# Kernel optimization log

Measured on AMD Instinct MI355X. Metric: run time of the kernel, lower is better.

## Reference

```python
import jax, jax.numpy as jnp
import numpy as np


def setup_inputs() -> dict:
    key = jax.random.key(0)
    ks = jax.random.split(key, 10)
    T, B, I, H, Z = 1024, 512, 128, 256, 1
    s = 0.1  # small init scale for stable recurrence
    return {
        "inputs": jax.random.normal(ks[0], (T, B, I), dtype=jnp.float32),
        "h0": jax.random.normal(ks[1], (B, H), dtype=jnp.float32) * s,
        "c0": jax.random.normal(ks[2], (B, H), dtype=jnp.float32) * s,
        "z0": jax.random.normal(ks[3], (B, Z), dtype=jnp.float32) * s,
        "W_ih": jax.random.normal(ks[4], (4 * H, I + Z), dtype=jnp.float32) * s,
        "W_hh": jax.random.normal(ks[5], (4 * H, H), dtype=jnp.float32) * s,
        "b_ih": jax.random.normal(ks[6], (4 * H,), dtype=jnp.float32) * s,
        "b_hh": jax.random.normal(ks[7], (4 * H,), dtype=jnp.float32) * s,
        "W_fc": jax.random.normal(ks[8], (Z, H), dtype=jnp.float32) * s,
        "b_fc": jax.random.normal(ks[9], (Z,), dtype=jnp.float32) * s,
    }


def reference(inputs, h0, c0, z0, W_ih, W_hh, b_ih, b_hh, W_fc, b_fc):
    def step(carry, x_t):
        h, c, z = carry
        xz = jnp.concatenate([x_t, z], axis=1)  # [B, I+Z]
        gates = xz @ W_ih.T + b_ih + h @ W_hh.T + b_hh  # [B, 4H]
        i_g, f_g, g_g, o_g = jnp.split(gates, 4, axis=1)  # torch gate order i,f,g,o
        i_g = jax.nn.sigmoid(i_g)
        f_g = jax.nn.sigmoid(f_g)
        g_g = jnp.tanh(g_g)
        o_g = jax.nn.sigmoid(o_g)
        c = f_g * c + i_g * g_g
        h = o_g * jnp.tanh(c)
        z = jnp.tanh(h @ W_fc.T + b_fc)  # [B, Z]
        return (h, c, z), z

    (h, c, _), outputs = jax.lax.scan(step, (h0, c0, z0), inputs)
    return outputs, h, c  # outputs: [T, B, Z]
```

## Files before the change

### kernel.cpp

```cpp
#include <hip/hip_runtime.h>
#include <hip/hip_bf16.h>
#include <stdint.h>

#define TT 1024
#define BB 512
#define II 128
#define HH 256
#define NKC 12
#define GSTR 132

typedef __attribute__((ext_vector_type(8))) short bf16x8;
typedef __attribute__((ext_vector_type(4))) float f32x4;
typedef __attribute__((ext_vector_type(4))) uint32_t u32x4;
typedef unsigned long long ull;

__device__ __forceinline__ float fsig(float x)  { return 1.0f / (1.0f + __expf(-x)); }
__device__ __forceinline__ float ftanh(float x) { return 1.0f - 2.0f / (__expf(2.0f * x) + 1.0f); }
__device__ __forceinline__ uint16_t f2bf(float f) {
    return __bfloat16_as_ushort(__float2bfloat16(f));
}
__device__ __forceinline__ float bf2lo(uint32_t w) { return __uint_as_float(w << 16); }
__device__ __forceinline__ float bf2hi(uint32_t w) { return __uint_as_float(w & 0xffff0000u); }

__global__ __launch_bounds__(512, 1) void lstm_kernel(
    const float* __restrict__ x,
    const float* __restrict__ h0, const float* __restrict__ c0,
    const float* __restrict__ z0,
    const float* __restrict__ W_ih, const float* __restrict__ W_hh,
    const float* __restrict__ b_ih, const float* __restrict__ b_hh,
    const float* __restrict__ Wfc, const float* __restrict__ bfc,
    uint32_t* __restrict__ hbF, uint32_t* __restrict__ hbS,
    float* __restrict__ out)
{
    __shared__ __align__(16) uint16_t a_sh[NKC * 4 * 16 * 8];
    __shared__ float g_sh[16 * GSTR];
    __shared__ float zp_sh[8 * 16];

    const int tid  = threadIdx.x;
    const int lane = tid & 63, wv = tid >> 6;
    const int bid  = blockIdx.x;
    const int mm   = bid >> 3;
    const int role = mm & 7, grp = (bid & 7) * 4 + (mm >> 3);
    const int b0   = grp * 16;
    const int arow = tid >> 5, auu = tid & 31;
    const int u_g  = role * 32 + auu;
    const int xc   = (tid & 31) * 4;
    const int grole = wv, grow = lane & 15, gwq = lane >> 4;

    bf16x8 wreg[NKC];
    {
        int lc = wv * 16 + (lane & 15);
        int col = (lc >> 5) * 256 + role * 32 + (lc & 31);
        #pragma unroll
        for (int kc = 0; kc < NKC; ++kc) {
            int k0 = kc * 32 + (lane >> 4) * 8;
            const float* src = (k0 < II) ? &W_ih[(size_t)col * (II + 1) + k0]
                                         : &W_hh[(size_t)col * HH + (k0 - II)];
            bf16x8 wv8;
            #pragma unroll
            for (int j = 0; j < 8; ++j) wv8[j] = (short)f2bf(src[j]);
            wreg[kc] = wv8;
        }
    }

    float bia[4], wzv[4];
    #pragma unroll
    for (int g = 0; g < 4; ++g) {
        int c = g * 256 + u_g;
        bia[g] = b_ih[c] + b_hh[c];
        wzv[g] = W_ih[(size_t)c * (II + 1) + II];
    }
    float wfc8[8];
    #pragma unroll
    for (int j = 0; j < 8; ++j) wfc8[j] = Wfc[grole * 32 + gwq * 8 + j];
    const float wfc  = Wfc[u_g];
    const float bfcs = bfc[0];
    const float z0r  = z0[b0 + arow];
    float c_r = c0[(size_t)(b0 + arow) * HH + u_g];

    {
        const float* hp = h0 + (size_t)(b0 + grow) * HH + grole * 32 + gwq * 8;
        uint4 pw;
        pw.x = (uint32_t)f2bf(hp[0]) | ((uint32_t)f2bf(hp[1]) << 16);
        pw.y = (uint32_t)f2bf(hp[2]) | ((uint32_t)f2bf(hp[3]) << 16);
        pw.z = (uint32_t)f2bf(hp[4]) | ((uint32_t)f2bf(hp[5]) << 16);
        pw.w = (uint32_t)f2bf(hp[6]) | ((uint32_t)f2bf(hp[7]) << 16);
        *(uint4*)&a_sh[(((4 + grole) * 4 + gwq) * 16 + grow) * 8] = pw;
    }
    {
        float4 xv = *(const float4*)&x[(size_t)(b0 + arow) * II + xc];
        int kcx = xc >> 5, gx = (xc >> 3) & 3, jx = xc & 7;
        ushort4 p;
        p.x = f2bf(xv.x); p.y = f2bf(xv.y); p.z = f2bf(xv.z); p.w = f2bf(xv.w);
        *(ushort4*)&a_sh[((kcx * 4 + gx) * 16 + arow) * 8 + jx] = p;
    }

    uint32_t strikes = 0;
    for (int t = 0; t <= TT; ++t) {
        float4 xn = make_float4(0.f, 0.f, 0.f, 0.f);
        if (t + 1 < TT)
            xn = *(const float4*)&x[(size_t)(t + 1) * (BB * II) + (size_t)(b0 + arow) * II + xc];

        if (t > 0 && grole != role) {
            const int par = (t - 1) & 1;
            const size_t gidx = ((((size_t)par * 32 + grp) * 8 + grole) * 16 + grow) * 16
                              + gwq * 4;
            const ull* pF = (const ull*)hbF + gidx;
            const ull* pS = (const ull*)hbS + gidx;
            u32x4 a0, a1;
            uint32_t it = 0;
            const uint32_t cap = (strikes >= 4) ? 64u : (1u << 20);
            const uint32_t tt = (uint32_t)t;
            for (;;) {
                u32x4 f0, f1;
                asm volatile(
                    "global_load_dwordx4 %0, %2, off sc0\n\t"
                    "global_load_dwordx4 %1, %2, off offset:16 sc0\n\t"
                    "s_waitcnt vmcnt(0)"
                    : "=&v"(f0), "=&v"(f1) : "v"(pF) : "memory");
                if (min(min(f0.y, f0.w), min(f1.y, f1.w)) >= tt) { a0 = f0; a1 = f1; break; }
                ++it;
                if ((it & 3) != 0) { __builtin_amdgcn_s_sleep(1); continue; }
                u32x4 s0, s1;
                asm volatile(
                    "global_load_dwordx4 %0, %2, off sc0 sc1\n\t"
                    "global_load_dwordx4 %1, %2, off offset:16 sc0 sc1\n\t"
                    "s_waitcnt vmcnt(0)"
                    : "=&v"(s0), "=&v"(s1) : "v"(pS) : "memory");
                if (min(min(s0.y, s0.w), min(s1.y, s1.w)) >= tt) { a0 = s0; a1 = s1; break; }
                __builtin_amdgcn_s_sleep(1);
                if (it > cap) { ++strikes; a0 = s0; a1 = s1; break; }
            }
            uint32_t w0 = a0.x, w1 = a0.z, w2 = a1.x, w3 = a1.z;
            uint4 pw; pw.x = w0; pw.y = w1; pw.z = w2; pw.w = w3;
            *(uint4*)&a_sh[(((4 + grole) * 4 + gwq) * 16 + grow) * 8] = pw;
            float p = bf2lo(w0) * wfc8[0] + bf2hi(w0) * wfc8[1]
                    + bf2lo(w1) * wfc8[2] + bf2hi(w1) * wfc8[3]
                    + bf2lo(w2) * wfc8[4] + bf2hi(w2) * wfc8[5]
                    + bf2lo(w3) * wfc8[6] + bf2hi(w3) * wfc8[7];
            p += __shfl_xor(p, 16, 64);
            p += __shfl_xor(p, 32, 64);
            if (gwq == 0) zp_sh[grole * 16 + grow] = p;
        }
        __syncthreads();

        if (t == TT) {
            if (role == 0 && tid < 16) {
                float s = bfcs;
                #pragma unroll
                for (int r = 0; r < 8; ++r) s += zp_sh[r * 16 + tid];
                out[(size_t)(TT - 1) * BB + b0 + tid] = ftanh(s);
            }
            break;
        }

        f32x4 acc0 = {0.f, 0.f, 0.f, 0.f}, acc1 = {0.f, 0.f, 0.f, 0.f};
        #pragma unroll
        for (int kc = 0; kc < NKC; kc += 2) {
            bf16x8 a0 = *(const bf16x8*)&a_sh[((kc * 4 + (lane >> 4)) * 16 + (lane & 15)) * 8];
            acc0 = __builtin_amdgcn_mfma_f32_16x16x32_bf16(a0, wreg[kc], acc0, 0, 0, 0);
            bf16x8 a1 = *(const bf16x8*)&a_sh[(((kc + 1) * 4 + (lane >> 4)) * 16 + (lane & 15)) * 8];
            acc1 = __builtin_amdgcn_mfma_f32_16x16x32_bf16(a1, wreg[kc + 1], acc1, 0, 0, 0);
        }
        f32x4 acc = acc0 + acc1;
        {
            int r0 = (lane >> 4) * 4, cb = wv * 16 + (lane & 15);
            #pragma unroll
            for (int i = 0; i < 4; ++i) g_sh[(r0 + i) * GSTR + cb] = acc[i];
        }
        __syncthreads();

        {
            int kcx = xc >> 5, gx = (xc >> 3) & 3, jx = xc & 7;
            ushort4 p;
            p.x = f2bf(xn.x); p.y = f2bf(xn.y); p.z = f2bf(xn.z); p.w = f2bf(xn.w);
            *(ushort4*)&a_sh[((kcx * 4 + gx) * 16 + arow) * 8 + jx] = p;
        }

        float zp_;
        if (t == 0) {
            zp_ = z0r;
        } else {
            float s = bfcs;
            #pragma unroll
            for (int r = 0; r < 8; ++r) s += zp_sh[r * 16 + arow];
            zp_ = ftanh(s);
            if (role == 0 && auu == 0)
                out[(size_t)(t - 1) * BB + b0 + arow] = zp_;
        }
        float gi = g_sh[arow * GSTR +      auu] + bia[0] + wzv[0] * zp_;
        float gf = g_sh[arow * GSTR + 32 + auu] + bia[1] + wzv[1] * zp_;
        float gg = g_sh[arow * GSTR + 64 + auu] + bia[2] + wzv[2] * zp_;
        float go = g_sh[arow * GSTR + 96 + auu] + bia[3] + wzv[3] * zp_;
        float ig = fsig(gi), fg = fsig(gf), gc = ftanh(gg), og = fsig(go);
        float cn = fg * c_r + ig * gc;
        c_r = cn;
        float hn = og * ftanh(cn);

        uint32_t hb16 = f2bf(hn);
        uint32_t nb = __shfl_down(hb16, 1, 64);
        if (!(auu & 1)) {
            uint32_t word = hb16 | (nb << 16);
            *(uint32_t*)&a_sh[(((4 + role) * 4 + (auu >> 3)) * 16 + arow) * 8 + (auu & 7)]
                = word;
            ull q = ((ull)(uint32_t)(t + 1) << 32) | (ull)word;
            size_t o = ((((size_t)(t & 1) * 32 + grp) * 8 + role) * 16 + arow) * 16
                     + (auu >> 1);
            asm volatile("global_store_dwordx2 %0, %1, off sc0"
                         :: "v"((ull*)hbF + o), "v"(q) : "memory");
            asm volatile("global_store_dwordx2 %0, %1, off sc0 sc1"
                         :: "v"((ull*)hbS + o), "v"(q) : "memory");
        }
        float pz = hn * wfc;
        #pragma unroll
        for (int off = 16; off >= 1; off >>= 1) pz += __shfl_xor(pz, off, 32);
        if (auu == 0) zp_sh[role * 16 + arow] = pz;

        if (t == TT - 1) {
            size_t ho = (size_t)TT * BB + (size_t)(b0 + arow) * HH + u_g;
            out[ho] = hn;
            out[ho + (size_t)BB * HH] = cn;
        }
    }
}

extern "C" void kernel_launch(void* const* d_in, const int* in_sizes, int n_in,
                              void* d_out, int out_size, void* d_ws, size_t ws_size,
                              hipStream_t stream) {
    const float* x    = (const float*)d_in[0];
    const float* h0   = (const float*)d_in[1];
    const float* c0   = (const float*)d_in[2];
    const float* z0   = (const float*)d_in[3];
    const float* W_ih = (const float*)d_in[4];
    const float* W_hh = (const float*)d_in[5];
    const float* b_ih = (const float*)d_in[6];
    const float* b_hh = (const float*)d_in[7];
    const float* Wfc  = (const float*)d_in[8];
    const float* bfc  = (const float*)d_in[9];
    float* out = (float*)d_out;

    const size_t COPY = (size_t)2 * 32 * 8 * 16 * 16 * 8;
    if (ws_size >= 2 * COPY) {
        uint32_t* hbF = (uint32_t*)d_ws;
        uint32_t* hbS = (uint32_t*)((char*)d_ws + COPY);
        hipMemsetAsync(d_ws, 0, 2 * COPY, stream);
        lstm_kernel<<<256, 512, 0, stream>>>(x, h0, c0, z0, W_ih, W_hh, b_ih, b_hh,
                                             Wfc, bfc, hbF, hbS, out);
    } else {
        uint32_t* hb = (uint32_t*)d_ws;
        hipMemsetAsync(d_ws, 0, COPY, stream);
        lstm_kernel<<<256, 512, 0, stream>>>(x, h0, c0, z0, W_ih, W_hh, b_ih, b_hh,
                                             Wfc, bfc, hb, hb, out);
    }
}
```

Measured before the change: 2.211 ms.

## Process two batch cohorts per block to overlap cross-block exchange latency

Halves the grid to 128 blocks, with each block handling two 16-row batch cohorts in alternating phases. Its weight registers are reused for both cohorts, so one cohort's compute can hide the other cohort's wait on cross-block hidden-state exchange. The global publish of h is also changed: after an extra barrier, one wave does 16-byte stores from shared memory instead of every even lane doing 8-byte stores. The cost is more barriers per step and serialized work per block, with fewer CUs in use.

Result: slower. 4.721 ms (+113.5%).

```diff
diff --git a/kernel.cpp b/kernel.cpp
--- a/kernel.cpp
+++ b/kernel.cpp
@@ -8,6 +8,7 @@
 #define HH 256
 #define NKC 12
 #define GSTR 132
+#define NGRP 16
 
 typedef __attribute__((ext_vector_type(8))) short bf16x8;
 typedef __attribute__((ext_vector_type(4))) float f32x4;
@@ -32,20 +33,20 @@
     uint32_t* __restrict__ hbF, uint32_t* __restrict__ hbS,
     float* __restrict__ out)
 {
-    __shared__ __align__(16) uint16_t a_sh[NKC * 4 * 16 * 8];
+    __shared__ __align__(16) uint16_t a_sh[2][NKC * 4 * 16 * 8];
     __shared__ float g_sh[16 * GSTR];
-    __shared__ float zp_sh[8 * 16];
+    __shared__ float zp_sh[2][8 * 16];
 
     const int tid  = threadIdx.x;
     const int lane = tid & 63, wv = tid >> 6;
     const int bid  = blockIdx.x;
-    const int mm   = bid >> 3;
-    const int role = mm & 7, grp = (bid & 7) * 4 + (mm >> 3);
-    const int b0   = grp * 16;
+    const int xcls = bid & 7, kk = bid >> 3;
+    const int grp  = xcls * 2 + (kk >> 3), role = kk & 7;
     const int arow = tid >> 5, auu = tid & 31;
     const int u_g  = role * 32 + auu;
     const int xc   = (tid & 31) * 4;
     const int grole = wv, grow = lane & 15, gwq = lane >> 4;
+    const int pr = lane & 15, pg = lane >> 4;
 
     bf16x8 wreg[NKC];
     {
@@ -75,153 +76,175 @@
     for (int j = 0; j < 8; ++j) wfc8[j] = Wfc[grole * 32 + gwq * 8 + j];
     const float wfc  = Wfc[u_g];
     const float bfcs = bfc[0];
-    const float z0r  = z0[b0 + arow];
-    float c_r = c0[(size_t)(b0 + arow) * HH + u_g];
-
-    {
-        const float* hp = h0 + (size_t)(b0 + grow) * HH + grole * 32 + gwq * 8;
+    const int b0A = grp * 32, b0B = grp * 32 + 16;
+    const float z0rA = z0[b0A + arow], z0rB = z0[b0B + arow];
+    float c_rA = c0[(size_t)(b0A + arow) * HH + u_g];
+    float c_rB = c0[(size_t)(b0B + arow) * HH + u_g];
+
+    #pragma unroll
+    for (int coh = 0; coh < 2; ++coh) {
+        const float* hp = h0 + (size_t)(grp * 32 + coh * 16 + grow) * HH
+                        + grole * 32 + gwq * 8;
         uint4 pw;
         pw.x = (uint32_t)f2bf(hp[0]) | ((uint32_t)f2bf(hp[1]) << 16);
         pw.y = (uint32_t)f2bf(hp[2]) | ((uint32_t)f2bf(hp[3]) << 16);
         pw.z = (uint32_t)f2bf(hp[4]) | ((uint32_t)f2bf(hp[5]) << 16);
         pw.w = (uint32_t)f2bf(hp[6]) | ((uint32_t)f2bf(hp[7]) << 16);
-        *(uint4*)&a_sh[(((4 + grole) * 4 + gwq) * 16 + grow) * 8] = pw;
-    }
-    {
-        float4 xv = *(const float4*)&x[(size_t)(b0 + arow) * II + xc];
+        *(uint4*)&a_sh[coh][(((4 + grole) * 4 + gwq) * 16 + grow) * 8] = pw;
+
+        float4 xv = *(const float4*)&x[(size_t)(grp * 32 + coh * 16 + arow) * II + xc];
         int kcx = xc >> 5, gx = (xc >> 3) & 3, jx = xc & 7;
         ushort4 p;
         p.x = f2bf(xv.x); p.y = f2bf(xv.y); p.z = f2bf(xv.z); p.w = f2bf(xv.w);
-        *(ushort4*)&a_sh[((kcx * 4 + gx) * 16 + arow) * 8 + jx] = p;
+        *(ushort4*)&a_sh[coh][((kcx * 4 + gx) * 16 + arow) * 8 + jx] = p;
     }
 
     uint32_t strikes = 0;
+
+#define PHASE(COH, B0, CR, Z0R)                                               \
+{                                                                             \
+    float4 xn = make_float4(0.f, 0.f, 0.f, 0.f);                              \
+    if (t + 1 < TT)                                                           \
+        xn = *(const float4*)&x[(size_t)(t + 1) * (BB * II)                   \
+                                + (size_t)((B0) + arow) * II + xc];           \
+    if (t > 0 && grole != role) {                                             \
+        const int par = (t - 1) & 1;                                          \
+        const size_t gidx = (((((size_t)par * NGRP + grp) * 2 + (COH)) * 8    \
+                              + grole) * 16 + grow) * 16 + gwq * 4;           \
+        const ull* pF = (const ull*)hbF + gidx;                               \
+        const ull* pS = (const ull*)hbS + gidx;                               \
+        u32x4 a0, a1;                                                         \
+        uint32_t it = 0;                                                      \
+        const uint32_t cap = (strikes >= 4) ? 64u : (1u << 20);               \
+        const uint32_t tt_ = (uint32_t)t;                                     \
+        for (;;) {                                                            \
+            u32x4 f0, f1;                                                     \
+            asm volatile("global_load_dwordx4 %0, %2, off sc0\n\t"            \
+                         "global_load_dwordx4 %1, %2, off offset:16 sc0\n\t"  \
+                         "s_waitcnt vmcnt(0)"                                 \
+                         : "=&v"(f0), "=&v"(f1) : "v"(pF) : "memory");        \
+            if (min(min(f0.y, f0.w), min(f1.y, f1.w)) >= tt_) {               \
+                a0 = f0; a1 = f1; break; }                                    \
+            ++it;                                                             \
+            if ((it & 3) != 0) { __builtin_amdgcn_s_sleep(1); continue; }     \
+            u32x4 s0, s1;                                                     \
+            asm volatile("global_load_dwordx4 %0, %2, off sc0 sc1\n\t"        \
+                         "global_load_dwordx4 %1, %2, off offset:16 sc0 sc1\n\t" \
+                         "s_waitcnt vmcnt(0)"                                 \
+                         : "=&v"(s0), "=&v"(s1) : "v"(pS) : "memory");        \
+            if (min(min(s0.y, s0.w), min(s1.y, s1.w)) >= tt_) {               \
+                a0 = s0; a1 = s1; break; }                                    \
+            __builtin_amdgcn_s_sleep(1);                                      \
+            if (it > cap) { ++strikes; a0 = s0; a1 = s1; break; }             \
+        }                                                                     \
+        uint32_t w0 = a0.x, w1 = a0.z, w2 = a1.x, w3 = a1.z;                  \
+        uint4 pw; pw.x = w0; pw.y = w1; pw.z = w2; pw.w = w3;                 \
+        *(uint4*)&a_sh[COH][(((4 + grole) * 4 + gwq) * 16 + grow) * 8] = pw;  \
+        float p = bf2lo(w0) * wfc8[0] + bf2hi(w0) * wfc8[1]                   \
+                + bf2lo(w1) * wfc8[2] + bf2hi(w1) * wfc8[3]                   \
+                + bf2lo(w2) * wfc8[4] + bf2hi(w2) * wfc8[5]                   \
+                + bf2lo(w3) * wfc8[6] + bf2hi(w3) * wfc8[7];                  \
+        p += __shfl_xor(p, 16, 64);                                           \
+        p += __shfl_xor(p, 32, 64);                                           \
+        if (gwq == 0) zp_sh[COH][grole * 16 + grow] = p;                      \
+    }                                                                         \
+    __syncthreads();                                                   \
+    if (t == TT) {                                                            \
+        if (role == 0 && tid < 16) {                                          \
+            float s = bfcs;                                                   \
+            _Pragma("unroll")                                                 \
+            for (int r = 0; r < 8; ++r) s += zp_sh[COH][r * 16 + tid];        \
+            out[(size_t)(TT - 1) * BB + (B0) + tid] = ftanh(s);               \
+        }                                                                     \
+    } else {                                                                  \
+        f32x4 acc0 = {0.f, 0.f, 0.f, 0.f}, acc1 = {0.f, 0.f, 0.f, 0.f};      \
+        _Pragma("unroll")                                                     \
+        for (int kc = 0; kc < NKC; kc += 2) {                                 \
+            bf16x8 aa0 = *(const bf16x8*)                                     \
+                &a_sh[COH][((kc * 4 + (lane >> 4)) * 16 + (lane & 15)) * 8];  \
+            acc0 = __builtin_amdgcn_mfma_f32_16x16x32_bf16(aa0, wreg[kc], acc0, 0, 0, 0); \
+            bf16x8 aa1 = *(const bf16x8*)                                     \
+                &a_sh[COH][(((kc + 1) * 4 + (lane >> 4)) * 16 + (lane & 15)) * 8]; \
+            acc1 = __builtin_amdgcn_mfma_f32_16x16x32_bf16(aa1, wreg[kc + 1], acc1, 0, 0, 0); \
+        }                                                                     \
+        f32x4 acc = acc0 + acc1;                                              \
+        {                                                                     \
+            int r0 = (lane >> 4) * 4, cb = wv * 16 + (lane & 15);             \
+            _Pragma("unroll")                                                 \
+            for (int i = 0; i < 4; ++i) g_sh[(r0 + i) * GSTR + cb] = acc[i];  \
+        }                                                                     \
+        __syncthreads();                                               \
+        {                                                                     \
+            int kcx = xc >> 5, gx = (xc >> 3) & 3, jx = xc & 7;               \
+            ushort4 p;                                                        \
+            p.x = f2bf(xn.x); p.y = f2bf(xn.y);                               \
+            p.z = f2bf(xn.z); p.w = f2bf(xn.w);                               \
+            *(ushort4*)&a_sh[COH][((kcx * 4 + gx) * 16 + arow) * 8 + jx] = p; \
+        }                                                                     \
+        float zp_;                                                            \
+        if (t == 0) { zp_ = (Z0R); }                                          \
+        else {                                                                \
+            float s = bfcs;                                                   \
+            _Pragma("unroll")                                                 \
+            for (int r = 0; r < 8; ++r) s += zp_sh[COH][r * 16 + arow];       \
+            zp_ = ftanh(s);                                                   \
+            if (role == 0 && auu == 0)                                        \
+                out[(size_t)(t - 1) * BB + (B0) + arow] = zp_;                \
+        }                                                                     \
+        float gi = g_sh[arow * GSTR +      auu] + bia[0] + wzv[0] * zp_;      \
+        float gf = g_sh[arow * GSTR + 32 + auu] + bia[1] + wzv[1] * zp_;      \
+        float gg = g_sh[arow * GSTR + 64 + auu] + bia[2] + wzv[2] * zp_;      \
+        float go = g_sh[arow * GSTR + 96 + auu] + bia[3] + wzv[3] * zp_;      \
+        float ig = fsig(gi), fg = fsig(gf), gc = ftanh(gg), og = fsig(go);    \
+        float cn = fg * (CR) + ig * gc;                                       \
+        (CR) = cn;                                                            \
+        float hn = og * ftanh(cn);                                            \
+        uint32_t hb16 = f2bf(hn);                                             \
+        uint32_t nb = __shfl_down(hb16, 1, 64);                               \
+        if (!(auu & 1)) {                                                     \
+            *(uint32_t*)&a_sh[COH][(((4 + role) * 4 + (auu >> 3)) * 16        \
+                                    + arow) * 8 + (auu & 7)]                  \
+                = hb16 | (nb << 16);                                          \
+        }                                                                     \
+        float pz = hn * wfc;                                                  \
+        _Pragma("unroll")                                                     \
+        for (int off = 16; off >= 1; off >>= 1)                               \
+            pz += __shfl_xor(pz, off, 32);                                    \
+        if (auu == 0) zp_sh[COH][role * 16 + arow] = pz;                      \
+        if (t == TT - 1) {                                                    \
+            size_t ho = (size_t)TT * BB + (size_t)((B0) + arow) * HH + u_g;   \
+            out[ho] = hn;                                                     \
+            out[ho + (size_t)BB * HH] = cn;                                   \
+        }                                                                     \
+        __syncthreads();                 \
+        if (wv == role) {                                                     \
+            uint4 hw = *(const uint4*)                                        \
+                &a_sh[COH][((4 + role) * 4 + pg) * 128 + pr * 8];             \
+            const uint32_t st = (uint32_t)(t + 1);                            \
+            u32x4 qa; qa.x = hw.x; qa.y = st; qa.z = hw.y; qa.w = st;         \
+            u32x4 qb; qb.x = hw.z; qb.y = st; qb.z = hw.w; qb.w = st;         \
+            const size_t widx = (((((size_t)(t & 1) * NGRP + grp) * 2         \
+                                   + (COH)) * 8 + role) * 16 + pr) * 16       \
+                              + pg * 4;                                       \
+            ull* pF = (ull*)hbF + widx;                                       \
+            ull* pS = (ull*)hbS + widx;                                       \
+            asm volatile("global_store_dwordx4 %0, %1, off sc0"               \
+                         :: "v"(pF), "v"(qa) : "memory");                     \
+            asm volatile("global_store_dwordx4 %0, %1, off offset:16 sc0"     \
+                         :: "v"(pF), "v"(qb) : "memory");                     \
+            asm volatile("global_store_dwordx4 %0, %1, off sc0 sc1"           \
+                         :: "v"(pS), "v"(qa) : "memory");                     \
+            asm volatile("global_store_dwordx4 %0, %1, off offset:16 sc0 sc1" \
+                         :: "v"(pS), "v"(qb) : "memory");                     \
+        }                                                                     \
+    }                                                                         \
+}
+
     for (int t = 0; t <= TT; ++t) {
-        float4 xn = make_float4(0.f, 0.f, 0.f, 0.f);
-        if (t + 1 < TT)
-            xn = *(const float4*)&x[(size_t)(t + 1) * (BB * II) + (size_t)(b0 + arow) * II + xc];
-
-        if (t > 0 && grole != role) {
-            const int par = (t - 1) & 1;
-            const size_t gidx = ((((size_t)par * 32 + grp) * 8 + grole) * 16 + grow) * 16
-                              + gwq * 4;
-            const ull* pF = (const ull*)hbF + gidx;
-            const ull* pS = (const ull*)hbS + gidx;
-            u32x4 a0, a1;
-            uint32_t it = 0;
-            const uint32_t cap = (strikes >= 4) ? 64u : (1u << 20);
-            const uint32_t tt = (uint32_t)t;
-            for (;;) {
-                u32x4 f0, f1;
-                asm volatile(
-                    "global_load_dwordx4 %0, %2, off sc0\n\t"
-                    "global_load_dwordx4 %1, %2, off offset:16 sc0\n\t"
-                    "s_waitcnt vmcnt(0)"
-                    : "=&v"(f0), "=&v"(f1) : "v"(pF) : "memory");
-                if (min(min(f0.y, f0.w), min(f1.y, f1.w)) >= tt) { a0 = f0; a1 = f1; break; }
-                ++it;
-                if ((it & 3) != 0) { __builtin_amdgcn_s_sleep(1); continue; }
-                u32x4 s0, s1;
-                asm volatile(
-                    "global_load_dwordx4 %0, %2, off sc0 sc1\n\t"
-                    "global_load_dwordx4 %1, %2, off offset:16 sc0 sc1\n\t"
-                    "s_waitcnt vmcnt(0)"
-                    : "=&v"(s0), "=&v"(s1) : "v"(pS) : "memory");
-                if (min(min(s0.y, s0.w), min(s1.y, s1.w)) >= tt) { a0 = s0; a1 = s1; break; }
-                __builtin_amdgcn_s_sleep(1);
-                if (it > cap) { ++strikes; a0 = s0; a1 = s1; break; }
-            }
-            uint32_t w0 = a0.x, w1 = a0.z, w2 = a1.x, w3 = a1.z;
-            uint4 pw; pw.x = w0; pw.y = w1; pw.z = w2; pw.w = w3;
-            *(uint4*)&a_sh[(((4 + grole) * 4 + gwq) * 16 + grow) * 8] = pw;
-            float p = bf2lo(w0) * wfc8[0] + bf2hi(w0) * wfc8[1]
-                    + bf2lo(w1) * wfc8[2] + bf2hi(w1) * wfc8[3]
-                    + bf2lo(w2) * wfc8[4] + bf2hi(w2) * wfc8[5]
-                    + bf2lo(w3) * wfc8[6] + bf2hi(w3) * wfc8[7];
-            p += __shfl_xor(p, 16, 64);
-            p += __shfl_xor(p, 32, 64);
-            if (gwq == 0) zp_sh[grole * 16 + grow] = p;
-        }
-        __syncthreads();
-
-        if (t == TT) {
-            if (role == 0 && tid < 16) {
-                float s = bfcs;
-                #pragma unroll
-                for (int r = 0; r < 8; ++r) s += zp_sh[r * 16 + tid];
-                out[(size_t)(TT - 1) * BB + b0 + tid] = ftanh(s);
-            }
-            break;
-        }
-
-        f32x4 acc0 = {0.f, 0.f, 0.f, 0.f}, acc1 = {0.f, 0.f, 0.f, 0.f};
-        #pragma unroll
-        for (int kc = 0; kc < NKC; kc += 2) {
-            bf16x8 a0 = *(const bf16x8*)&a_sh[((kc * 4 + (lane >> 4)) * 16 + (lane & 15)) * 8];
-            acc0 = __builtin_amdgcn_mfma_f32_16x16x32_bf16(a0, wreg[kc], acc0, 0, 0, 0);
-            bf16x8 a1 = *(const bf16x8*)&a_sh[(((kc + 1) * 4 + (lane >> 4)) * 16 + (lane & 15)) * 8];
-            acc1 = __builtin_amdgcn_mfma_f32_16x16x32_bf16(a1, wreg[kc + 1], acc1, 0, 0, 0);
-        }
-        f32x4 acc = acc0 + acc1;
-        {
-            int r0 = (lane >> 4) * 4, cb = wv * 16 + (lane & 15);
-            #pragma unroll
-            for (int i = 0; i < 4; ++i) g_sh[(r0 + i) * GSTR + cb] = acc[i];
-        }
-        __syncthreads();
-
-        {
-            int kcx = xc >> 5, gx = (xc >> 3) & 3, jx = xc & 7;
-            ushort4 p;
-            p.x = f2bf(xn.x); p.y = f2bf(xn.y); p.z = f2bf(xn.z); p.w = f2bf(xn.w);
-            *(ushort4*)&a_sh[((kcx * 4 + gx) * 16 + arow) * 8 + jx] = p;
-        }
-
-        float zp_;
-        if (t == 0) {
-            zp_ = z0r;
-        } else {
-            float s = bfcs;
-            #pragma unroll
-            for (int r = 0; r < 8; ++r) s += zp_sh[r * 16 + arow];
-            zp_ = ftanh(s);
-            if (role == 0 && auu == 0)
-                out[(size_t)(t - 1) * BB + b0 + arow] = zp_;
-        }
-        float gi = g_sh[arow * GSTR +      auu] + bia[0] + wzv[0] * zp_;
-        float gf = g_sh[arow * GSTR + 32 + auu] + bia[1] + wzv[1] * zp_;
-        float gg = g_sh[arow * GSTR + 64 + auu] + bia[2] + wzv[2] * zp_;
-        float go = g_sh[arow * GSTR + 96 + auu] + bia[3] + wzv[3] * zp_;
-        float ig = fsig(gi), fg = fsig(gf), gc = ftanh(gg), og = fsig(go);
-        float cn = fg * c_r + ig * gc;
-        c_r = cn;
-        float hn = og * ftanh(cn);
-
-        uint32_t hb16 = f2bf(hn);
-        uint32_t nb = __shfl_down(hb16, 1, 64);
-        if (!(auu & 1)) {
-            uint32_t word = hb16 | (nb << 16);
-            *(uint32_t*)&a_sh[(((4 + role) * 4 + (auu >> 3)) * 16 + arow) * 8 + (auu & 7)]
-                = word;
-            ull q = ((ull)(uint32_t)(t + 1) << 32) | (ull)word;
-            size_t o = ((((size_t)(t & 1) * 32 + grp) * 8 + role) * 16 + arow) * 16
-                     + (auu >> 1);
-            asm volatile("global_store_dwordx2 %0, %1, off sc0"
-                         :: "v"((ull*)hbF + o), "v"(q) : "memory");
-            asm volatile("global_store_dwordx2 %0, %1, off sc0 sc1"
-                         :: "v"((ull*)hbS + o), "v"(q) : "memory");
-        }
-        float pz = hn * wfc;
-        #pragma unroll
-        for (int off = 16; off >= 1; off >>= 1) pz += __shfl_xor(pz, off, 32);
-        if (auu == 0) zp_sh[role * 16 + arow] = pz;
-
-        if (t == TT - 1) {
-            size_t ho = (size_t)TT * BB + (size_t)(b0 + arow) * HH + u_g;
-            out[ho] = hn;
-            out[ho + (size_t)BB * HH] = cn;
-        }
-    }
+        PHASE(0, b0A, c_rA, z0rA)
+        PHASE(1, b0B, c_rB, z0rB)
+    }
+#undef PHASE
 }
 
 extern "C" void kernel_launch(void* const* d_in, const int* in_sizes, int n_in,
@@ -239,17 +262,17 @@
     const float* bfc  = (const float*)d_in[9];
     float* out = (float*)d_out;
 
-    const size_t COPY = (size_t)2 * 32 * 8 * 16 * 16 * 8;
+    const size_t COPY = (size_t)2 * NGRP * 2 * 8 * 16 * 16 * 8;
     if (ws_size >= 2 * COPY) {
         uint32_t* hbF = (uint32_t*)d_ws;
         uint32_t* hbS = (uint32_t*)((char*)d_ws + COPY);
         hipMemsetAsync(d_ws, 0, 2 * COPY, stream);
-        lstm_kernel<<<256, 512, 0, stream>>>(x, h0, c0, z0, W_ih, W_hh, b_ih, b_hh,
+        lstm_kernel<<<128, 512, 0, stream>>>(x, h0, c0, z0, W_ih, W_hh, b_ih, b_hh,
                                              Wfc, bfc, hbF, hbS, out);
     } else {
         uint32_t* hb = (uint32_t*)d_ws;
         hipMemsetAsync(d_ws, 0, COPY, stream);
-        lstm_kernel<<<256, 512, 0, stream>>>(x, h0, c0, z0, W_ih, W_hh, b_ih, b_hh,
+        lstm_kernel<<<128, 512, 0, stream>>>(x, h0, c0, z0, W_ih, W_hh, b_ih, b_hh,
                                              Wfc, bfc, hb, hb, out);
     }
 }
```
